# Optimization experiments

Hardware: AMD Instinct MI355X
Metric: run time of the kernel (lower is better)

Reference implementation:

```python
import jax, jax.numpy as jnp
import numpy as np


def setup_inputs() -> dict:
    key = jax.random.key(0)
    ks = jax.random.split(key, 8)
    B, C, H, K, Wd, D = 4, 2048, 14, 80, 300, 1024
    s = 0.02  # weight init scale
    return {
        "img_feat": jax.random.normal(ks[0], (B, C, H, H), jnp.float32),
        "word_feat": jax.random.normal(ks[1], (K, Wd), jnp.float32),
        "W1": jax.random.normal(ks[2], (D, C), jnp.float32) * s,
        "W2": jax.random.normal(ks[3], (D, Wd), jnp.float32) * s,
        "W3": jax.random.normal(ks[4], (D, D), jnp.float32) * s,
        "b3": jnp.zeros((D,), jnp.float32),
        "W4": jax.random.normal(ks[5], (1, D), jnp.float32) * s,
        "b4": jnp.zeros((1,), jnp.float32),
    }


def reference(img_feat, word_feat, W1, W2, W3, b3, W4, b4):
    B, C, H, W = img_feat.shape
    x = jnp.transpose(img_feat, (0, 2, 3, 1))            # (B,H,W,C)
    iproj = jnp.einsum('bhwc,dc->bhwd', x, W1)           # fc1, no bias
    wproj = jnp.einsum('kv,dv->kd', word_feat, W2)       # fc2, no bias
    # bilinear interaction + tanh: (B,H,W,K,D)
    inter = jnp.tanh(iproj[:, :, :, None, :] * wproj[None, None, None, :, :])
    feat = jnp.einsum('bhwkd,ed->bhwke', inter, W3) + b3  # fc3
    coef = jnp.einsum('bhwkd,od->bhwko', feat, W4)[..., 0] + b4[0]  # (B,H,W,K)
    # softmax over the spatial positions (H*W) independently per class
    flat = coef.reshape(B, H * W, coef.shape[-1])
    sm = jax.nn.softmax(flat, axis=1).reshape(B, H, W, coef.shape[-1])  # (B,H,W,K)
    # broadcast-multiply: (B,H,W,K,C)
    fwc = x[:, :, :, None, :] * sm[..., None]
    semantic = jnp.sum(fwc, axis=(1, 2))                 # (B,K,C)
    return semantic, fwc, sm
```

## Files before the change

kernel.cpp:

```cpp
#include <hip/hip_runtime.h>
#include <hip/hip_bf16.h>

#define B_   4
#define C_   2048
#define HH_  14
#define HW_  196
#define P_   784
#define PPAD_ 832
#define K_   80
#define WD_  300
#define D_   1024

typedef float f32x4_t __attribute__((ext_vector_type(4)));
typedef short s16x8  __attribute__((ext_vector_type(8)));
typedef float f32x4a __attribute__((ext_vector_type(4)));
typedef unsigned short u16;
typedef u16 u16x4 __attribute__((ext_vector_type(4)));
typedef u16 u16x8 __attribute__((ext_vector_type(8)));

#define XT_OFF    0
#define XTB_OFF   (XT_OFF + P_*C_)
#define W1B_OFF   (XTB_OFF + (PPAD_*C_)/2)
#define IPROJ_OFF (W1B_OFF + (D_*C_)/2)
#define W2TS_OFF  (IPROJ_OFF + P_*D_)
#define WPS_OFF   (W2TS_OFF + WD_*D_)
#define VD2_OFF   (WPS_OFF + K_*D_)
#define VD2P_OFF  (VD2_OFF + D_)
#define COEF_OFF  (VD2P_OFF + 32*D_)

static __device__ __forceinline__ u16 f2bf(float x) {
  __hip_bfloat16 h = __float2bfloat16(x);
  return *(u16*)&h;
}

#define PREP_BLOCKS 4296
__launch_bounds__(256)
__global__ void k_prep(const float* __restrict__ img, const float* __restrict__ W1,
                       const float* __restrict__ W2, const float* __restrict__ W3,
                       const float* __restrict__ W4,
                       float* __restrict__ xt, u16* __restrict__ xtb,
                       u16* __restrict__ w1b, float* __restrict__ w2ts,
                       float* __restrict__ vd2p) {
  __shared__ float tile[32][33];
  const int bid = blockIdx.x;
  const int t = threadIdx.x;
  if (bid < 2048) {
    int i = bid*256 + t;
    f32x4_t v = *(const f32x4_t*)&W1[(size_t)i*4];
    u16x4 o = { f2bf(v.x), f2bf(v.y), f2bf(v.z), f2bf(v.w) };
    *(u16x4*)&w1b[(size_t)i*4] = o;
  } else if (bid < 3840) {
    int r = bid - 2048;
    int c0 = (r & 63) * 32;
    int hw0 = ((r >> 6) % 7) * 32;
    int b = r / 448;
    int tx = t & 31, ty = t >> 5;
    #pragma unroll
    for (int i = 0; i < 4; i++) {
      int c = c0 + ty + i*8, hw = hw0 + tx;
      float v = 0.f;
      if (hw < HW_) v = img[((size_t)b*C_ + c)*HW_ + hw];
      tile[ty + i*8][tx] = v;
    }
    __syncthreads();
    #pragma unroll
    for (int i = 0; i < 4; i++) {
      int hw = hw0 + ty + i*8, c = c0 + tx;
      if (hw < HW_) {
        float v = tile[tx][ty + i*8];
        size_t idx = ((size_t)(b*HW_ + hw))*C_ + c;
        xt[idx] = v;
        xtb[idx] = f2bf(v);
      }
    }
  } else if (bid < 4160) {
    int r = bid - 3840;
    int d0 = (r & 31) * 32;
    int v0 = (r >> 5) * 32;
    int tx = t & 31, ty = t >> 5;
    #pragma unroll
    for (int i = 0; i < 4; i++) {
      int d = d0 + ty + i*8, v = v0 + tx;
      float val = 0.f;
      if (v < WD_) val = W2[(size_t)d*WD_ + v];
      tile[ty + i*8][tx] = val;
    }
    __syncthreads();
    const float s = 2.8853900817779268f;
    #pragma unroll
    for (int i = 0; i < 4; i++) {
      int v = v0 + ty + i*8, d = d0 + tx;
      if (v < WD_) w2ts[(size_t)v*D_ + d] = tile[tx][ty + i*8] * s;
    }
  } else if (bid < 4288) {
    int r = bid - 4160;
    int d = (r & 3) * 256 + t;
    int e0 = (r >> 2) * 32;
    float acc = 0.f;
    #pragma unroll
    for (int q = 0; q < 32; q++)
      acc = fmaf(W4[e0 + q], W3[(size_t)(e0 + q)*D_ + d], acc);
    vd2p[(size_t)(r >> 2)*D_ + d] = acc;
  } else {
    int r = bid - 4288;
    u16x8 z = {0,0,0,0,0,0,0,0};
    #pragma unroll
    for (int i = 0; i < 6; i++) {
      size_t o = (size_t)P_*C_ + ((size_t)(r*256 + t)*6 + i)*8;
      *(u16x8*)&xtb[o] = z;
    }
  }
}

#define GK_ 256
#define MID_BLOCKS 289
__launch_bounds__(256, 2)
__global__ void k_mid(const u16* __restrict__ xtb, const u16* __restrict__ w1b,
                      const float* __restrict__ wf, const float* __restrict__ w2ts,
                      const float* __restrict__ vd2p,
                      float* __restrict__ iproj, float* __restrict__ wps,
                      float* __restrict__ vd2) {
  __shared__ __align__(16) char smem[2*64*GK_*2];
  const int bid = blockIdx.x;
  const int t = threadIdx.x;
  if (bid < 208) {
    u16* As = (u16*)smem;
    u16* Bs = As + 64*GK_;
    const int m0 = (bid >> 4) * 64, n0 = (bid & 15) * 64;
    const int wid = t >> 6, lane = t & 63;
    const int wm = wid >> 1, wn = wid & 1;
    const int lm = lane & 15, jr = lane >> 4;
    int offA[8], offB[8];
    u16* ldsA[8]; u16* ldsB[8];
    #pragma unroll
    for (int i = 0; i < 8; i++) {
      int c = i*256 + t;
      int row = c >> 5, js = c & 31;
      int j = js ^ (row & 7);
      offA[i] = (m0 + row) * C_ + j*8;
      offB[i] = (n0 + row) * C_ + j*8;
      ldsA[i] = &As[c*8];
      ldsB[i] = &Bs[c*8];
    }
    f32x4a acc[2][2] = {};
    for (int k0 = 0; k0 < C_; k0 += GK_) {
      #pragma unroll
      for (int i = 0; i < 8; i++)
        __builtin_amdgcn_global_load_lds((const __attribute__((address_space(1))) void*)(xtb + offA[i] + k0),
                                         (__attribute__((address_space(3))) void*)ldsA[i], 16, 0, 0);
      #pragma unroll
      for (int i = 0; i < 8; i++)
        __builtin_amdgcn_global_load_lds((const __attribute__((address_space(1))) void*)(w1b + offB[i] + k0),
                                         (__attribute__((address_space(3))) void*)ldsB[i], 16, 0, 0);
      __syncthreads();
      #pragma unroll
      for (int kk = 0; kk < 8; kk++) {
        int jx = ((kk*4 + jr) ^ (lm & 7)) * 8;
        s16x8 a0 = *(const s16x8*)&As[(wm*32 + lm)*GK_ + jx];
        s16x8 a1 = *(const s16x8*)&As[(wm*32 + 16 + lm)*GK_ + jx];
        s16x8 b0 = *(const s16x8*)&Bs[(wn*32 + lm)*GK_ + jx];
        s16x8 b1 = *(const s16x8*)&Bs[(wn*32 + 16 + lm)*GK_ + jx];
        acc[0][0] = __builtin_amdgcn_mfma_f32_16x16x32_bf16(a0, b0, acc[0][0], 0, 0, 0);
        acc[0][1] = __builtin_amdgcn_mfma_f32_16x16x32_bf16(a0, b1, acc[0][1], 0, 0, 0);
        acc[1][0] = __builtin_amdgcn_mfma_f32_16x16x32_bf16(a1, b0, acc[1][0], 0, 0, 0);
        acc[1][1] = __builtin_amdgcn_mfma_f32_16x16x32_bf16(a1, b1, acc[1][1], 0, 0, 0);
      }
      __syncthreads();
    }
    #pragma unroll
    for (int mi = 0; mi < 2; mi++)
      #pragma unroll
      for (int ni = 0; ni < 2; ni++)
        #pragma unroll
        for (int q = 0; q < 4; q++) {
          int prow = m0 + wm*32 + mi*16 + (lane>>4)*4 + q;
          int ncol = n0 + wn*32 + ni*16 + lm;
          if (prow < P_) iproj[(size_t)prow*D_ + ncol] = acc[mi][ni][q];
        }
  } else if (bid < 288) {
    float* wrow = (float*)smem;
    const int k = bid - 208;
    for (int i = t; i < WD_; i += 256) wrow[i] = wf[k*WD_ + i];
    __syncthreads();
    float4 acc = {0.f,0.f,0.f,0.f};
    const float4* w4 = (const float4*)w2ts;
    for (int v = 0; v < WD_; v++) {
      float s = wrow[v];
      float4 w = w4[(size_t)v*(D_/4) + t];
      acc.x = fmaf(s, w.x, acc.x); acc.y = fmaf(s, w.y, acc.y);
      acc.z = fmaf(s, w.z, acc.z); acc.w = fmaf(s, w.w, acc.w);
    }
    ((float4*)wps)[k*(D_/4) + t] = acc;
  } else {
    #pragma unroll
    for (int j = 0; j < 4; j++) {
      int d = j*256 + t;
      float s = 0.f;
      #pragma unroll
      for (int q = 0; q < 32; q++) s += vd2p[(size_t)q*D_ + d];
      vd2[d] = -2.0f * s;
    }
  }
}

__launch_bounds__(320)
__global__ void k_coef(const float* __restrict__ iproj, const float* __restrict__ wps,
                       const float* __restrict__ vd2, float* __restrict__ coef) {
  __shared__ float ipd[D_];
  __shared__ float v2s[D_];
  const int p = blockIdx.x;
  const int t = threadIdx.x;
  for (int i = t; i < D_; i += 320) {
    ipd[i] = iproj[(size_t)p*D_ + i];
    v2s[i] = vd2[i];
  }
  __syncthreads();
  const int k = t >> 2, dq = t & 3;
  const float4* wv  = (const float4*)&wps[(size_t)k*D_ + dq*256];
  const float4* ip4 = (const float4*)&ipd[dq*256];
  const float4* v24 = (const float4*)&v2s[dq*256];
  float acc = 0.f;
  for (int q = 0; q < 64; q++) {
    float4 w  = wv[q];
    float4 ip = ip4[q];
    float4 v2 = v24[q];
    float r0 = __builtin_amdgcn_rcpf(__builtin_amdgcn_exp2f(ip.x*w.x) + 1.0f);
    float r1 = __builtin_amdgcn_rcpf(__builtin_amdgcn_exp2f(ip.y*w.y) + 1.0f);
    float r2 = __builtin_amdgcn_rcpf(__builtin_amdgcn_exp2f(ip.z*w.z) + 1.0f);
    float r3 = __builtin_amdgcn_rcpf(__builtin_amdgcn_exp2f(ip.w*w.w) + 1.0f);
    acc = fmaf(v2.x, r0, acc);
    acc = fmaf(v2.y, r1, acc);
    acc = fmaf(v2.z, r2, acc);
    acc = fmaf(v2.w, r3, acc);
  }
  acc += __shfl_xor(acc, 1);
  acc += __shfl_xor(acc, 2);
  if (dq == 0) coef[(size_t)p*K_ + k] = acc;
}

__global__ void k_softmax(const float* __restrict__ coef, float* __restrict__ sm) {
  int bk = blockIdx.x; int b = bk / K_, k = bk % K_;
  int t = threadIdx.x;
  float v[4]; float mx = -1e30f;
  #pragma unroll
  for (int i = 0; i < 4; i++) {
    int hw = t + i*64;
    v[i] = (hw < HW_) ? coef[(size_t)(b*HW_ + hw)*K_ + k] : -1e30f;
    mx = fmaxf(mx, v[i]);
  }
  #pragma unroll
  for (int off = 32; off > 0; off >>= 1) mx = fmaxf(mx, __shfl_xor(mx, off));
  float e[4]; float sum = 0.f;
  #pragma unroll
  for (int i = 0; i < 4; i++) {
    int hw = t + i*64;
    e[i] = (hw < HW_) ? __builtin_amdgcn_exp2f((v[i]-mx)*1.4426950408889634f) : 0.f;
    sum += e[i];
  }
  #pragma unroll
  for (int off = 32; off > 0; off >>= 1) sum += __shfl_xor(sum, off);
  float rs = 1.0f / sum;
  #pragma unroll
  for (int i = 0; i < 4; i++) {
    int hw = t + i*64;
    if (hw < HW_) sm[(size_t)(b*HW_ + hw)*K_ + k] = e[i]*rs;
  }
}

#define SEM_BLOCKS 32
#define FWC_BLOCKS 2048
__launch_bounds__(256)
__global__ void k_fwc_sem(const float* __restrict__ xt, const float* __restrict__ sm,
                          float* __restrict__ fwc, float* __restrict__ semantic) {
  const int bid = blockIdx.x;
  const int t = threadIdx.x;
  if (bid < SEM_BLOCKS) {
    const int b = bid >> 3;
    const int c = (bid & 7) * 256 + t;
    float acc[K_];
    #pragma unroll
    for (int k = 0; k < K_; k++) acc[k] = 0.f;
    const float* smb = sm + (size_t)b*HW_*K_;
    const float* xb  = xt + (size_t)b*HW_*C_ + c;
    for (int hw = 0; hw < HW_; hw++) {
      float xv = xb[(size_t)hw*C_];
      #pragma unroll
      for (int k4 = 0; k4 < K_/4; k4++) {
        f32x4_t sv = *(const f32x4_t*)&smb[hw*K_ + k4*4];
        acc[k4*4+0] = fmaf(xv, sv.x, acc[k4*4+0]);
        acc[k4*4+1] = fmaf(xv, sv.y, acc[k4*4+1]);
        acc[k4*4+2] = fmaf(xv, sv.z, acc[k4*4+2]);
        acc[k4*4+3] = fmaf(xv, sv.w, acc[k4*4+3]);
      }
    }
    #pragma unroll
    for (int k = 0; k < K_; k++)
      semantic[((size_t)(b*K_ + k))*C_ + c] = acc[k];
  } else {
    const size_t N4 = (size_t)P_*K_*(C_/4);
    const size_t stride4 = (size_t)FWC_BLOCKS*256;
    size_t i4 = (size_t)(bid - SEM_BLOCKS)*256 + t;
    for (; i4 < N4; i4 += stride4) {
      int c4 = (int)(i4 & (C_/4 - 1));
      int pk = (int)(i4 >> 9);
      int p  = pk / K_;
      float s = sm[pk];
      f32x4_t xv = *(const f32x4_t*)&xt[(size_t)p*C_ + c4*4];
      __builtin_nontemporal_store(xv * s, (f32x4_t*)&fwc[i4*4]);
    }
  }
}

extern "C" void kernel_launch(void* const* d_in, const int* in_sizes, int n_in,
                              void* d_out, int out_size, void* d_ws, size_t ws_size,
                              hipStream_t stream) {
  const float* img  = (const float*)d_in[0];
  const float* wf   = (const float*)d_in[1];
  const float* W1   = (const float*)d_in[2];
  const float* W2   = (const float*)d_in[3];
  const float* W3   = (const float*)d_in[4];
  const float* W4   = (const float*)d_in[6];

  float* out = (float*)d_out;
  float* semantic = out;
  float* fwc      = out + (size_t)B_*K_*C_;
  float* sm       = fwc + (size_t)P_*K_*C_;

  float* ws    = (float*)d_ws;
  float* xt    = ws + XT_OFF;
  u16*   xtb   = (u16*)(ws + XTB_OFF);
  u16*   w1b   = (u16*)(ws + W1B_OFF);
  float* iproj = ws + IPROJ_OFF;
  float* w2ts  = ws + W2TS_OFF;
  float* wps   = ws + WPS_OFF;
  float* vd2   = ws + VD2_OFF;
  float* vd2p  = ws + VD2P_OFF;
  float* coef  = ws + COEF_OFF;

  k_prep<<<PREP_BLOCKS, 256, 0, stream>>>(img, W1, W2, W3, W4, xt, xtb, w1b, w2ts, vd2p);
  k_mid<<<MID_BLOCKS, 256, 0, stream>>>(xtb, w1b, wf, w2ts, vd2p, iproj, wps, vd2);
  k_coef<<<P_, 320, 0, stream>>>(iproj, wps, vd2, coef);
  k_softmax<<<B_*K_, 64, 0, stream>>>(coef, sm);
  k_fwc_sem<<<SEM_BLOCKS + FWC_BLOCKS, 256, 0, stream>>>(xt, sm, fwc, semantic);
}
```

Baseline: 183.1 us.

## Fuse semantic reduction into softmax kernel, split fwc into its own kernel

Moves the semantic (B,K,C) reduction out of the fwc kernel and into the softmax kernel. Each softmax block keeps its normalized row in shared memory and reduces over all 2048 channels with vectorized loads. Previously only 32 blocks did this reduction, each holding 80 accumulators per thread. Now 320 blocks each produce one class row, which spreads the work wider and removes the long tail from the fwc kernel. In exchange, each 64-thread block streams the whole xt slice for its batch, so xt is re-read 80 times from cache.

Result: slower. 435.2 us (+137.7%).

```diff
diff --git a/kernel.cpp b/kernel.cpp
--- a/kernel.cpp
+++ b/kernel.cpp
@@ -238,7 +238,10 @@
   if (dq == 0) coef[(size_t)p*K_ + k] = acc;
 }
 
-__global__ void k_softmax(const float* __restrict__ coef, float* __restrict__ sm) {
+__launch_bounds__(64)
+__global__ void k_softmax_sem(const float* __restrict__ coef, const float* __restrict__ xt,
+                              float* __restrict__ sm, float* __restrict__ semantic) {
+  __shared__ float srow[HW_];
   int bk = blockIdx.x; int b = bk / K_, k = bk % K_;
   int t = threadIdx.x;
   float v[4]; float mx = -1e30f;
@@ -263,51 +266,50 @@
   #pragma unroll
   for (int i = 0; i < 4; i++) {
     int hw = t + i*64;
-    if (hw < HW_) sm[(size_t)(b*HW_ + hw)*K_ + k] = e[i]*rs;
-  }
-}
-
-#define SEM_BLOCKS 32
+    if (hw < HW_) {
+      float s = e[i]*rs;
+      sm[(size_t)(b*HW_ + hw)*K_ + k] = s;
+      srow[hw] = s;
+    }
+  }
+  __syncthreads();
+  f32x4_t acc[8];
+  #pragma unroll
+  for (int j = 0; j < 8; j++) acc[j] = (f32x4_t){0.f,0.f,0.f,0.f};
+  const float* xb = xt + (size_t)b*HW_*C_;
+  for (int hw = 0; hw < HW_; hw++) {
+    float s = srow[hw];
+    const float* xr = xb + (size_t)hw*C_ + t*4;
+    #pragma unroll
+    for (int j = 0; j < 8; j++) {
+      f32x4_t xv = *(const f32x4_t*)(xr + j*256);
+      acc[j].x = fmaf(xv.x, s, acc[j].x);
+      acc[j].y = fmaf(xv.y, s, acc[j].y);
+      acc[j].z = fmaf(xv.z, s, acc[j].z);
+      acc[j].w = fmaf(xv.w, s, acc[j].w);
+    }
+  }
+  float* so = semantic + ((size_t)(b*K_ + k))*C_ + t*4;
+  #pragma unroll
+  for (int j = 0; j < 8; j++)
+    *(f32x4_t*)(so + j*256) = acc[j];
+}
+
 #define FWC_BLOCKS 2048
 __launch_bounds__(256)
-__global__ void k_fwc_sem(const float* __restrict__ xt, const float* __restrict__ sm,
-                          float* __restrict__ fwc, float* __restrict__ semantic) {
-  const int bid = blockIdx.x;
+__global__ void k_fwc(const float* __restrict__ xt, const float* __restrict__ sm,
+                      float* __restrict__ fwc) {
   const int t = threadIdx.x;
-  if (bid < SEM_BLOCKS) {
-    const int b = bid >> 3;
-    const int c = (bid & 7) * 256 + t;
-    float acc[K_];
-    #pragma unroll
-    for (int k = 0; k < K_; k++) acc[k] = 0.f;
-    const float* smb = sm + (size_t)b*HW_*K_;
-    const float* xb  = xt + (size_t)b*HW_*C_ + c;
-    for (int hw = 0; hw < HW_; hw++) {
-      float xv = xb[(size_t)hw*C_];
-      #pragma unroll
-      for (int k4 = 0; k4 < K_/4; k4++) {
-        f32x4_t sv = *(const f32x4_t*)&smb[hw*K_ + k4*4];
-        acc[k4*4+0] = fmaf(xv, sv.x, acc[k4*4+0]);
-        acc[k4*4+1] = fmaf(xv, sv.y, acc[k4*4+1]);
-        acc[k4*4+2] = fmaf(xv, sv.z, acc[k4*4+2]);
-        acc[k4*4+3] = fmaf(xv, sv.w, acc[k4*4+3]);
-      }
-    }
-    #pragma unroll
-    for (int k = 0; k < K_; k++)
-      semantic[((size_t)(b*K_ + k))*C_ + c] = acc[k];
-  } else {
-    const size_t N4 = (size_t)P_*K_*(C_/4);
-    const size_t stride4 = (size_t)FWC_BLOCKS*256;
-    size_t i4 = (size_t)(bid - SEM_BLOCKS)*256 + t;
-    for (; i4 < N4; i4 += stride4) {
-      int c4 = (int)(i4 & (C_/4 - 1));
-      int pk = (int)(i4 >> 9);
-      int p  = pk / K_;
-      float s = sm[pk];
-      f32x4_t xv = *(const f32x4_t*)&xt[(size_t)p*C_ + c4*4];
-      __builtin_nontemporal_store(xv * s, (f32x4_t*)&fwc[i4*4]);
-    }
+  const size_t N4 = (size_t)P_*K_*(C_/4);
+  const size_t stride4 = (size_t)FWC_BLOCKS*256;
+  size_t i4 = (size_t)blockIdx.x*256 + t;
+  for (; i4 < N4; i4 += stride4) {
+    int c4 = (int)(i4 & (C_/4 - 1));
+    int pk = (int)(i4 >> 9);
+    int p  = pk / K_;
+    float s = sm[pk];
+    f32x4_t xv = *(const f32x4_t*)&xt[(size_t)p*C_ + c4*4];
+    __builtin_nontemporal_store(xv * s, (f32x4_t*)&fwc[i4*4]);
   }
 }
 
@@ -340,6 +342,6 @@
   k_prep<<<PREP_BLOCKS, 256, 0, stream>>>(img, W1, W2, W3, W4, xt, xtb, w1b, w2ts, vd2p);
   k_mid<<<MID_BLOCKS, 256, 0, stream>>>(xtb, w1b, wf, w2ts, vd2p, iproj, wps, vd2);
   k_coef<<<P_, 320, 0, stream>>>(iproj, wps, vd2, coef);
-  k_softmax<<<B_*K_, 64, 0, stream>>>(coef, sm);
-  k_fwc_sem<<<SEM_BLOCKS + FWC_BLOCKS, 256, 0, stream>>>(xt, sm, fwc, semantic);
-}
+  k_softmax_sem<<<B_*K_, 64, 0, stream>>>(coef, xt, sm, semantic);
+  k_fwc<<<FWC_BLOCKS, 256, 0, stream>>>(xt, sm, fwc);
+}
```
